# Performance work log

Measured on AMD Instinct MI355X. Metric: run time of the kernel, lower is better.

Reference implementation:

```python
import jax, jax.numpy as jnp
import numpy as np

B, T, C, H = 4, 2048, 768, 64

def setup_inputs() -> dict:
    key = jax.random.key(0)
    kx, kq, kk, kv = jax.random.split(key, 4)
    x = jax.random.normal(kx, (B, T, C), dtype=jnp.float32)
    # torch Linear(C->H, bias=False): y = x @ W with W [C, H]
    s = 1.0 / np.sqrt(C)
    Wq = jax.random.normal(kq, (C, H), dtype=jnp.float32) * s
    Wk = jax.random.normal(kk, (C, H), dtype=jnp.float32) * s
    Wv = jax.random.normal(kv, (C, H), dtype=jnp.float32) * s
    return {"x": x, "Wq": Wq, "Wk": Wk, "Wv": Wv}

def reference(x, Wq, Wk, Wv):
    Bx, Tx, Cx = x.shape
    q = jnp.einsum('btc,ch->bth', x, Wq)
    k = jnp.einsum('btc,ch->bth', x, Wk)
    v = jnp.einsum('btc,ch->bth', x, Wv)
    # NOTE: original scales by C**-0.5 (n_embeddings), not head_size**-0.5
    w = jnp.einsum('bqh,bkh->bqk', q, k) * (Cx ** -0.5)  # [B, T, T]
    causal = jnp.tril(jnp.ones((Tx, Tx), dtype=bool))
    w = jnp.where(causal, w, -jnp.inf)
    w = jax.nn.softmax(w, axis=-1)
    # dropout: eval mode (identity)
    out = jnp.einsum('bqk,bkh->bqh', w, v)  # [B, T, H]
    return out
```

## Files before the change

### kernel.cpp

```cpp
#include <hip/hip_runtime.h>
#include <math.h>

#define TB 2048
#define CB 768
#define NB 4
#define NROWS (NB * TB)
#define NSMAX 16
#define WGPB 136

typedef __attribute__((ext_vector_type(8))) short bf16x8;
typedef __attribute__((ext_vector_type(4))) float f32x4;
typedef __attribute__((ext_vector_type(2))) float f32x2;
typedef __attribute__((ext_vector_type(2))) unsigned int u32x2;
typedef __attribute__((ext_vector_type(4))) unsigned int u32x4;

__device__ inline unsigned short f2bf(float f) {
  union { float f; unsigned u; } v; v.f = f;
  unsigned r = v.u + 0x7FFFu + ((v.u >> 16) & 1u);
  return (unsigned short)(r >> 16);
}
__device__ inline unsigned pack2bf(float a, float b) {
  return (unsigned)f2bf(a) | ((unsigned)f2bf(b) << 16);
}
__device__ inline float bf2f(unsigned short u) {
  union { unsigned u; float f; } v; v.u = (unsigned)u << 16; return v.f;
}

__global__ void cvt_w_kernel(const float* __restrict__ Wq, const float* __restrict__ Wk,
                             const float* __restrict__ Wv, unsigned short* __restrict__ Wt) {
  __shared__ float tw[64][65];
  const float* W = (blockIdx.y == 0) ? Wq : (blockIdx.y == 1) ? Wk : Wv;
  const int c0 = blockIdx.x * 64;
  const int row = threadIdx.x >> 2, seg = threadIdx.x & 3;
#pragma unroll
  for (int i = 0; i < 4; ++i) {
    float4 f = *(const float4*)(W + (size_t)(c0 + row) * 64 + seg * 16 + i * 4);
    tw[row][seg * 16 + i * 4 + 0] = f.x;
    tw[row][seg * 16 + i * 4 + 1] = f.y;
    tw[row][seg * 16 + i * 4 + 2] = f.z;
    tw[row][seg * 16 + i * 4 + 3] = f.w;
  }
  __syncthreads();
  const int j = threadIdx.x >> 2, cq = threadIdx.x & 3;
  unsigned short* dst = Wt + (size_t)(blockIdx.y * 64 + j) * CB + c0 + cq * 16;
  u32x4 ua, ub;
#pragma unroll
  for (int i = 0; i < 4; ++i) ua[i] = pack2bf(tw[cq * 16 + 2 * i][j], tw[cq * 16 + 2 * i + 1][j]);
#pragma unroll
  for (int i = 0; i < 4; ++i) ub[i] = pack2bf(tw[cq * 16 + 8 + 2 * i][j], tw[cq * 16 + 9 + 2 * i][j]);
  *(u32x4*)dst = ua;
  *(u32x4*)(dst + 8) = ub;
}

__launch_bounds__(256)
__global__ void proj_direct_kernel(const float* __restrict__ x,
                                   const unsigned short* __restrict__ Wt,
                                   unsigned short* __restrict__ q,
                                   unsigned short* __restrict__ k,
                                   unsigned short* __restrict__ vT) {
  __shared__ __align__(16) unsigned short xs[16 * 64];
  __shared__ float tr[64][17];
  const int tid = threadIdx.x;
  const int wv = tid >> 6;
  const int l = tid & 63;
  const int lrow = l & 15, lg = l >> 4;
  const int m0 = blockIdx.x * 16;
  const int srow = tid >> 4;
  const int sq = tid & 15;
  const float* xp = x + (size_t)(m0 + srow) * CB + sq * 4;
  const int swz = (srow & 7) << 4;

  f32x4 acc[3];
#pragma unroll
  for (int n = 0; n < 3; ++n) acc[n] = (f32x4){0.f, 0.f, 0.f, 0.f};

  float4 f = *(const float4*)xp;
  for (int k0 = 0; k0 < CB; k0 += 64) {
    {
      u32x2 c;
      c.x = pack2bf(f.x, f.y);
      c.y = pack2bf(f.z, f.w);
      *(u32x2*)((char*)xs + srow * 128 + ((sq * 8) ^ swz)) = c;
    }
    if (k0 + 64 < CB) f = *(const float4*)(xp + k0 + 64);
    __syncthreads();

#pragma unroll
    for (int s = 0; s < 2; ++s) {
      bf16x8 af = *(const bf16x8*)((const char*)xs + lrow * 128 +
                                   ((s * 64 + lg * 16) ^ ((lrow & 7) << 4)));
#pragma unroll
      for (int nf = 0; nf < 3; ++nf) {
        int col = wv * 48 + nf * 16 + lrow;
        bf16x8 bfr = *(const bf16x8*)(Wt + (size_t)col * CB + k0 + s * 32 + lg * 8);
        acc[nf] = __builtin_amdgcn_mfma_f32_16x16x32_bf16(af, bfr, acc[nf], 0, 0, 0);
      }
    }
    __syncthreads();
  }

#pragma unroll
  for (int nf = 0; nf < 3; ++nf) {
    int j = wv * 48 + nf * 16 + lrow;
#pragma unroll
    for (int r = 0; r < 4; ++r) {
      int grow = m0 + lg * 4 + r;
      if (j < 64)       q[(size_t)grow * 64 + j] = f2bf(acc[nf][r]);
      else if (j < 128) k[(size_t)grow * 64 + (j - 64)] = f2bf(acc[nf][r]);
      else              tr[j - 128][lg * 4 + r] = acc[nf][r];
    }
  }
  __syncthreads();
  {
    const int b = m0 >> 11, t0 = m0 & (TB - 1);
    const int h = tid >> 2, tq = tid & 3;
    u32x2 pk;
    pk.x = pack2bf(tr[h][tq * 4 + 0], tr[h][tq * 4 + 1]);
    pk.y = pack2bf(tr[h][tq * 4 + 2], tr[h][tq * 4 + 3]);
    *(u32x2*)(vT + ((size_t)(b * 64 + h)) * TB + t0 + tq * 4) = pk;
  }
}

__launch_bounds__(512)
__global__ void attn_kernel(const unsigned short* __restrict__ q,
                            const unsigned short* __restrict__ k,
                            const unsigned short* __restrict__ vT,
                            unsigned short* __restrict__ PO, float* __restrict__ Mp,
                            float* __restrict__ Lp) {
  __shared__ __align__(16) char ksm[2][8192];
  __shared__ __align__(16) char vsm[2][8192];
  const int tid = threadIdx.x;
  const int wid = tid >> 6, l = tid & 63;
  const int lrow = l & 15, lg = l >> 4;
  const int b = blockIdx.y;
  const int w = blockIdx.x;

  int g = (int)((sqrtf((float)(8 * w + 1)) - 1.f) * 0.5f);
  while ((g + 1) * (g + 2) / 2 <= w) ++g;
  while (g * (g + 1) / 2 > w) --g;
  const int b128 = w - g * (g + 1) / 2;
  const int kv0a = b128 * 128, kv0b = kv0a + 64;
  const int t = 8 * g + wid;
  const int q0w = t * 16;
  const int qrow = q0w + lrow;

  const unsigned short* qb = q + (size_t)b * TB * 64;
  const char* kbb = (const char*)(k + (size_t)b * TB * 64);
  const unsigned short* vb = vT + (size_t)b * 64 * TB;

  const int srow = tid >> 3;
  const int sc = (tid & 7) * 16;
  const int kswz_w = (srow & 7) << 4;
  const int vswz_w = (srow & 3) << 5;
  float4 ka = *(const float4*)(kbb + (size_t)kv0a * 128 + tid * 16);
  float4 kb2 = *(const float4*)(kbb + (size_t)kv0b * 128 + tid * 16);
  float4 va = *(const float4*)((const char*)(vb + (size_t)srow * TB + kv0a) + sc);
  float4 vb2 = *(const float4*)((const char*)(vb + (size_t)srow * TB + kv0b) + sc);

  bf16x8 qf[2];
#pragma unroll
  for (int s = 0; s < 2; ++s)
    qf[s] = *(const bf16x8*)(qb + (size_t)qrow * 64 + s * 32 + lg * 8);

  *(float4*)(ksm[0] + srow * 128 + (sc ^ kswz_w)) = ka;
  *(float4*)(ksm[1] + srow * 128 + (sc ^ kswz_w)) = kb2;
  *(float4*)(vsm[0] + srow * 128 + (sc ^ vswz_w)) = va;
  *(float4*)(vsm[1] + srow * 128 + (sc ^ vswz_w)) = vb2;
  __syncthreads();

  const int kswz = (lrow & 7) << 4;
  const float scale = 0.03608439182435161f;
  const bool useb = (kv0b <= q0w + 15);

  f32x4 S0[4];
#pragma unroll
  for (int cf = 0; cf < 4; ++cf) S0[cf] = (f32x4){0.f, 0.f, 0.f, 0.f};
#pragma unroll
  for (int cf = 0; cf < 4; ++cf) {
    const char* kp = ksm[0] + (cf * 16 + lrow) * 128;
#pragma unroll
    for (int s = 0; s < 2; ++s) {
      bf16x8 kf = *(const bf16x8*)(kp + ((s * 64 + lg * 16) ^ kswz));
      S0[cf] = __builtin_amdgcn_mfma_f32_16x16x32_bf16(kf, qf[s], S0[cf], 0, 0, 0);
    }
  }
  float tmx = -INFINITY;
  {
    const bool msk = (kv0a + 63 > q0w);
#pragma unroll
    for (int cf = 0; cf < 4; ++cf)
#pragma unroll
      for (int r = 0; r < 4; ++r) {
        float vv = S0[cf][r] * scale;
        if (msk) {
          int kvi = kv0a + cf * 16 + lg * 4 + r;
          vv = (kvi > qrow) ? -INFINITY : vv;
        }
        S0[cf][r] = vv;
        tmx = fmaxf(tmx, vv);
      }
  }
  f32x4 S1[4];
  if (useb) {
#pragma unroll
    for (int cf = 0; cf < 4; ++cf) S1[cf] = (f32x4){0.f, 0.f, 0.f, 0.f};
#pragma unroll
    for (int cf = 0; cf < 4; ++cf) {
      const char* kp = ksm[1] + (cf * 16 + lrow) * 128;
#pragma unroll
      for (int s = 0; s < 2; ++s) {
        bf16x8 kf = *(const bf16x8*)(kp + ((s * 64 + lg * 16) ^ kswz));
        S1[cf] = __builtin_amdgcn_mfma_f32_16x16x32_bf16(kf, qf[s], S1[cf], 0, 0, 0);
      }
    }
    const bool msk = (kv0b + 63 > q0w);
#pragma unroll
    for (int cf = 0; cf < 4; ++cf)
#pragma unroll
      for (int r = 0; r < 4; ++r) {
        float vv = S1[cf][r] * scale;
        if (msk) {
          int kvi = kv0b + cf * 16 + lg * 4 + r;
          vv = (kvi > qrow) ? -INFINITY : vv;
        }
        S1[cf][r] = vv;
        tmx = fmaxf(tmx, vv);
      }
  }
  tmx = fmaxf(tmx, __shfl_xor(tmx, 16));
  tmx = fmaxf(tmx, __shfl_xor(tmx, 32));

  float lsl = 0.f;
  f32x4 o[4];
#pragma unroll
  for (int hf = 0; hf < 4; ++hf) o[hf] = (f32x4){0.f, 0.f, 0.f, 0.f};
  const int rswz = (lrow & 3) << 5;

  {
    float p[4][4];
#pragma unroll
    for (int cf = 0; cf < 4; ++cf)
#pragma unroll
      for (int r = 0; r < 4; ++r) {
        float pe = __expf(S0[cf][r] - tmx);
        p[cf][r] = pe;
        lsl += pe;
      }
    union { unsigned u[4]; bf16x8 v; } pbu[2];
#pragma unroll
    for (int s = 0; s < 2; ++s) {
      pbu[s].u[0] = pack2bf(p[2 * s][0], p[2 * s][1]);
      pbu[s].u[1] = pack2bf(p[2 * s][2], p[2 * s][3]);
      pbu[s].u[2] = pack2bf(p[2 * s + 1][0], p[2 * s + 1][1]);
      pbu[s].u[3] = pack2bf(p[2 * s + 1][2], p[2 * s + 1][3]);
    }
#pragma unroll
    for (int s = 0; s < 2; ++s)
#pragma unroll
      for (int hf = 0; hf < 4; ++hf) {
        int r = hf * 16 + lrow;
        int a1 = r * 128 + ((s * 64 + lg * 8) ^ rswz);
        u32x2 lo = *(const u32x2*)(vsm[0] + a1);
        u32x2 hi = *(const u32x2*)(vsm[0] + (a1 ^ 32));
        union { unsigned u[4]; bf16x8 v; } vfu;
        vfu.u[0] = lo.x; vfu.u[1] = lo.y; vfu.u[2] = hi.x; vfu.u[3] = hi.y;
        o[hf] = __builtin_amdgcn_mfma_f32_16x16x32_bf16(vfu.v, pbu[s].v, o[hf], 0, 0, 0);
      }
  }
  if (useb) {
    float p[4][4];
#pragma unroll
    for (int cf = 0; cf < 4; ++cf)
#pragma unroll
      for (int r = 0; r < 4; ++r) {
        float pe = __expf(S1[cf][r] - tmx);
        p[cf][r] = pe;
        lsl += pe;
      }
    union { unsigned u[4]; bf16x8 v; } pbu[2];
#pragma unroll
    for (int s = 0; s < 2; ++s) {
      pbu[s].u[0] = pack2bf(p[2 * s][0], p[2 * s][1]);
      pbu[s].u[1] = pack2bf(p[2 * s][2], p[2 * s][3]);
      pbu[s].u[2] = pack2bf(p[2 * s + 1][0], p[2 * s + 1][1]);
      pbu[s].u[3] = pack2bf(p[2 * s + 1][2], p[2 * s + 1][3]);
    }
#pragma unroll
    for (int s = 0; s < 2; ++s)
#pragma unroll
      for (int hf = 0; hf < 4; ++hf) {
        int r = hf * 16 + lrow;
        int a1 = r * 128 + ((s * 64 + lg * 8) ^ rswz);
        u32x2 lo = *(const u32x2*)(vsm[1] + a1);
        u32x2 hi = *(const u32x2*)(vsm[1] + (a1 ^ 32));
        union { unsigned u[4]; bf16x8 v; } vfu;
        vfu.u[0] = lo.x; vfu.u[1] = lo.y; vfu.u[2] = hi.x; vfu.u[3] = hi.y;
        o[hf] = __builtin_amdgcn_mfma_f32_16x16x32_bf16(vfu.v, pbu[s].v, o[hf], 0, 0, 0);
      }
  }

  float ls = lsl;
  ls += __shfl_xor(ls, 16);
  ls += __shfl_xor(ls, 32);

  size_t rowg = (size_t)b128 * NROWS + b * TB + qrow;
  unsigned short* pop = PO + rowg * 64 + lg * 4;
#pragma unroll
  for (int hf = 0; hf < 4; ++hf) {
    u32x2 pk;
    pk.x = pack2bf(o[hf][0], o[hf][1]);
    pk.y = pack2bf(o[hf][2], o[hf][3]);
    *(u32x2*)(pop + hf * 16) = pk;
  }
  if (lg == 0) {
    Mp[rowg] = tmx;
    Lp[rowg] = ls;
  }
}

__global__ void attn_reduce_kernel(const unsigned short* __restrict__ PO,
                                   const float* __restrict__ Mp,
                                   const float* __restrict__ Lp,
                                   float* __restrict__ out) {
  int id = blockIdx.x * 256 + threadIdx.x;
  if (id >= NROWS * 32) return;
  int row = id >> 5, h0 = (id & 31) * 2;
  int t = row & (TB - 1);
  int ns = (t >> 7) + 1;
  float M = -INFINITY;
#pragma unroll 4
  for (int s = 0; s < ns; ++s) M = fmaxf(M, Mp[(size_t)s * NROWS + row]);
  float L = 0.f, a0 = 0.f, a1 = 0.f;
#pragma unroll 4
  for (int s = 0; s < ns; ++s) {
    float w = __expf(Mp[(size_t)s * NROWS + row] - M);
    L += Lp[(size_t)s * NROWS + row] * w;
    unsigned pv = *(const unsigned*)(PO + ((size_t)s * NROWS + row) * 64 + h0);
    a0 += bf2f((unsigned short)(pv & 0xffff)) * w;
    a1 += bf2f((unsigned short)(pv >> 16)) * w;
  }
  float rL = 1.f / L;
  f32x2 r; r.x = a0 * rL; r.y = a1 * rL;
  *(f32x2*)(out + (size_t)row * 64 + h0) = r;
}

extern "C" void kernel_launch(void* const* d_in, const int* in_sizes, int n_in,
                              void* d_out, int out_size, void* d_ws, size_t ws_size,
                              hipStream_t stream) {
  const float* x  = (const float*)d_in[0];
  const float* Wq = (const float*)d_in[1];
  const float* Wk = (const float*)d_in[2];
  const float* Wv = (const float*)d_in[3];
  float* out = (float*)d_out;

  unsigned short* Wt = (unsigned short*)d_ws;
  unsigned short* qb = Wt + 192 * CB;
  unsigned short* kb = qb + (size_t)NROWS * 64;
  unsigned short* vT = kb + (size_t)NROWS * 64;
  char* scratch = (char*)(vT + (size_t)NROWS * 64);

  unsigned short* PO = (unsigned short*)scratch;
  float* Mp = (float*)(scratch + (size_t)NSMAX * NROWS * 64 * 2);
  float* Lp = Mp + (size_t)NSMAX * NROWS;

  hipLaunchKernelGGL(cvt_w_kernel, dim3(12, 3), dim3(256), 0, stream,
                     Wq, Wk, Wv, Wt);
  hipLaunchKernelGGL(proj_direct_kernel, dim3(NROWS / 16), dim3(256), 0, stream,
                     x, Wt, qb, kb, vT);
  hipLaunchKernelGGL(attn_kernel, dim3(WGPB, NB), dim3(512), 0, stream,
                     qb, kb, vT, PO, Mp, Lp);
  hipLaunchKernelGGL(attn_reduce_kernel, dim3((NROWS * 32) / 256), dim3(256), 0, stream,
                     PO, Mp, Lp, out);
}
```

Baseline: 50.92 us.

## Double-buffer projection x tile with 128-wide K steps and one barrier

The QKV projection kernel now stages x in two shared-memory buffers of 128 columns each instead of one 64-column buffer. Each thread loads 8 floats per step, and the loop runs 6 iterations instead of 12. Alternating buffers lets the trailing __syncthreads be dropped, halving the barrier count and the number of global-load/convert rounds. The cost is more shared memory and longer register live ranges. The projection is only part of the total kernel time.

```diff
diff --git a/kernel.cpp b/kernel.cpp
--- a/kernel.cpp
+++ b/kernel.cpp
@@ -58,7 +58,7 @@
                                    unsigned short* __restrict__ q,
                                    unsigned short* __restrict__ k,
                                    unsigned short* __restrict__ vT) {
-  __shared__ __align__(16) unsigned short xs[16 * 64];
+  __shared__ __align__(16) unsigned short xs[2][16 * 128];
   __shared__ float tr[64][17];
   const int tid = threadIdx.x;
   const int wv = tid >> 6;
@@ -66,29 +66,35 @@
   const int lrow = l & 15, lg = l >> 4;
   const int m0 = blockIdx.x * 16;
   const int srow = tid >> 4;
-  const int sq = tid & 15;
-  const float* xp = x + (size_t)(m0 + srow) * CB + sq * 4;
+  const int seg = tid & 15;
+  const float* xp = x + (size_t)(m0 + srow) * CB + seg * 8;
   const int swz = (srow & 7) << 4;
+  const int rswz = (lrow & 7) << 4;
 
   f32x4 acc[3];
 #pragma unroll
   for (int n = 0; n < 3; ++n) acc[n] = (f32x4){0.f, 0.f, 0.f, 0.f};
 
-  float4 f = *(const float4*)xp;
-  for (int k0 = 0; k0 < CB; k0 += 64) {
+  float4 f0 = *(const float4*)xp;
+  float4 f1 = *(const float4*)(xp + 4);
+  for (int it = 0; it < 6; ++it) {
+    const int k0 = it * 128;
     {
-      u32x2 c;
-      c.x = pack2bf(f.x, f.y);
-      c.y = pack2bf(f.z, f.w);
-      *(u32x2*)((char*)xs + srow * 128 + ((sq * 8) ^ swz)) = c;
-    }
-    if (k0 + 64 < CB) f = *(const float4*)(xp + k0 + 64);
+      u32x4 c;
+      c[0] = pack2bf(f0.x, f0.y); c[1] = pack2bf(f0.z, f0.w);
+      c[2] = pack2bf(f1.x, f1.y); c[3] = pack2bf(f1.z, f1.w);
+      *(u32x4*)((char*)xs[it & 1] + srow * 256 + ((seg * 16) ^ swz)) = c;
+    }
+    if (it < 5) {
+      f0 = *(const float4*)(xp + (it + 1) * 128);
+      f1 = *(const float4*)(xp + (it + 1) * 128 + 4);
+    }
     __syncthreads();
 
-#pragma unroll
-    for (int s = 0; s < 2; ++s) {
-      bf16x8 af = *(const bf16x8*)((const char*)xs + lrow * 128 +
-                                   ((s * 64 + lg * 16) ^ ((lrow & 7) << 4)));
+    const char* xb = (const char*)xs[it & 1];
+#pragma unroll
+    for (int s = 0; s < 4; ++s) {
+      bf16x8 af = *(const bf16x8*)(xb + lrow * 256 + ((s * 64 + lg * 16) ^ rswz));
 #pragma unroll
       for (int nf = 0; nf < 3; ++nf) {
         int col = wv * 48 + nf * 16 + lrow;
@@ -96,7 +102,6 @@
         acc[nf] = __builtin_amdgcn_mfma_f32_16x16x32_bf16(af, bfr, acc[nf], 0, 0, 0);
       }
     }
-    __syncthreads();
   }
 
 #pragma unroll
```

Result: no change. 51.55 us (+1.2%).

## Fuse split-KV reduction into attention kernel via last-block atomic counter

Applied to the files above, without the earlier changes.

Removes the separate reduction kernel. Each attention workgroup bumps a per-(batch, query-group) atomic counter after writing its partials, and the last workgroup to arrive merges all KV-split partials for its 128 rows and writes the final output. This saves one kernel launch and lets the merge overlap with other workgroups still computing. In exchange it adds a memset launch, threadfences and an atomic per workgroup, and the merge is serialized onto whichever block finishes last for each group.

```diff
diff --git a/kernel.cpp b/kernel.cpp
--- a/kernel.cpp
+++ b/kernel.cpp
@@ -126,9 +126,11 @@
                             const unsigned short* __restrict__ k,
                             const unsigned short* __restrict__ vT,
                             unsigned short* __restrict__ PO, float* __restrict__ Mp,
-                            float* __restrict__ Lp) {
+                            float* __restrict__ Lp, int* __restrict__ cnt,
+                            float* __restrict__ out) {
   __shared__ __align__(16) char ksm[2][8192];
   __shared__ __align__(16) char vsm[2][8192];
+  __shared__ int lastflag;
   const int tid = threadIdx.x;
   const int wid = tid >> 6, l = tid & 63;
   const int lrow = l & 15, lg = l >> 4;
@@ -316,32 +318,51 @@
     Mp[rowg] = tmx;
     Lp[rowg] = ls;
   }
-}
-
-__global__ void attn_reduce_kernel(const unsigned short* __restrict__ PO,
-                                   const float* __restrict__ Mp,
-                                   const float* __restrict__ Lp,
-                                   float* __restrict__ out) {
-  int id = blockIdx.x * 256 + threadIdx.x;
-  if (id >= NROWS * 32) return;
-  int row = id >> 5, h0 = (id & 31) * 2;
-  int t = row & (TB - 1);
-  int ns = (t >> 7) + 1;
-  float M = -INFINITY;
-#pragma unroll 4
-  for (int s = 0; s < ns; ++s) M = fmaxf(M, Mp[(size_t)s * NROWS + row]);
-  float L = 0.f, a0 = 0.f, a1 = 0.f;
-#pragma unroll 4
-  for (int s = 0; s < ns; ++s) {
-    float w = __expf(Mp[(size_t)s * NROWS + row] - M);
-    L += Lp[(size_t)s * NROWS + row] * w;
-    unsigned pv = *(const unsigned*)(PO + ((size_t)s * NROWS + row) * 64 + h0);
-    a0 += bf2f((unsigned short)(pv & 0xffff)) * w;
-    a1 += bf2f((unsigned short)(pv >> 16)) * w;
-  }
-  float rL = 1.f / L;
-  f32x2 r; r.x = a0 * rL; r.y = a1 * rL;
-  *(f32x2*)(out + (size_t)row * 64 + h0) = r;
+
+  __threadfence();
+  if (tid == 0) {
+    int old = atomicAdd(&cnt[b * 16 + g], 1);
+    lastflag = (old == g) ? 1 : 0;
+  }
+  __syncthreads();
+  if (lastflag) {
+    __threadfence();
+    const int row = 128 * g + (tid >> 2);
+    const int h0 = (tid & 3) * 16;
+    const size_t rbase = (size_t)b * TB + row;
+    float M = -INFINITY;
+    for (int s = 0; s <= g; ++s) M = fmaxf(M, Mp[(size_t)s * NROWS + rbase]);
+    float L = 0.f;
+    float a0[8], a1v[8];
+#pragma unroll
+    for (int i = 0; i < 8; ++i) { a0[i] = 0.f; a1v[i] = 0.f; }
+    for (int s = 0; s <= g; ++s) {
+      size_t rg = (size_t)s * NROWS + rbase;
+      float wgt = __expf(Mp[rg] - M);
+      L += Lp[rg] * wgt;
+      const unsigned short* pp = PO + rg * 64 + h0;
+      u32x4 pv0 = *(const u32x4*)pp;
+      u32x4 pv1 = *(const u32x4*)(pp + 8);
+#pragma unroll
+      for (int i = 0; i < 4; ++i) {
+        a0[2 * i]     += bf2f((unsigned short)(pv0[i] & 0xffff)) * wgt;
+        a0[2 * i + 1] += bf2f((unsigned short)(pv0[i] >> 16)) * wgt;
+        a1v[2 * i]     += bf2f((unsigned short)(pv1[i] & 0xffff)) * wgt;
+        a1v[2 * i + 1] += bf2f((unsigned short)(pv1[i] >> 16)) * wgt;
+      }
+    }
+    float rL = 1.f / L;
+    float* op = out + rbase * 64 + h0;
+    f32x4 r;
+    r.x = a0[0] * rL; r.y = a0[1] * rL; r.z = a0[2] * rL; r.w = a0[3] * rL;
+    *(f32x4*)op = r;
+    r.x = a0[4] * rL; r.y = a0[5] * rL; r.z = a0[6] * rL; r.w = a0[7] * rL;
+    *(f32x4*)(op + 4) = r;
+    r.x = a1v[0] * rL; r.y = a1v[1] * rL; r.z = a1v[2] * rL; r.w = a1v[3] * rL;
+    *(f32x4*)(op + 8) = r;
+    r.x = a1v[4] * rL; r.y = a1v[5] * rL; r.z = a1v[6] * rL; r.w = a1v[7] * rL;
+    *(f32x4*)(op + 12) = r;
+  }
 }
 
 extern "C" void kernel_launch(void* const* d_in, const int* in_sizes, int n_in,
@@ -362,13 +383,13 @@
   unsigned short* PO = (unsigned short*)scratch;
   float* Mp = (float*)(scratch + (size_t)NSMAX * NROWS * 64 * 2);
   float* Lp = Mp + (size_t)NSMAX * NROWS;
-
+  int* cnt = (int*)(Lp + (size_t)NSMAX * NROWS);
+
+  hipMemsetAsync(cnt, 0, NB * 16 * sizeof(int), stream);
   hipLaunchKernelGGL(cvt_w_kernel, dim3(12, 3), dim3(256), 0, stream,
                      Wq, Wk, Wv, Wt);
   hipLaunchKernelGGL(proj_direct_kernel, dim3(NROWS / 16), dim3(256), 0, stream,
                      x, Wt, qb, kb, vT);
   hipLaunchKernelGGL(attn_kernel, dim3(WGPB, NB), dim3(512), 0, stream,
-                     qb, kb, vT, PO, Mp, Lp);
-  hipLaunchKernelGGL(attn_reduce_kernel, dim3((NROWS * 32) / 256), dim3(256), 0, stream,
-                     PO, Mp, Lp, out);
-}
+                     qb, kb, vT, PO, Mp, Lp, cnt, out);
+}
```

Measured after the change: 199.8 us. 3.92x slower.
